# Kernel optimization log

Hardware: AMD Instinct MI355X
Metric: run time of the kernel (lower is better)

The kernel has to match this reference:

```python
import jax, jax.numpy as jnp
import numpy as np

W_, H_, D_ = 45, 30, 13
TEXT = 226
NVID = W_ * H_ * D_            # 17550 video tokens
L = TEXT + NVID                # 17776 total tokens
BLK = 128
NKEEP = 32
NBLK = (L + BLK - 1) // BLK    # 139 blocks
LPAD = NBLK * BLK              # 17792
LEVELS = (1, 2, 4, 8)
MASK_RATIOS = ((1, 0.0, 0.05), (2, 0.05, 0.15), (4, 0.15, 0.25), (8, 0.25, 0.5), (0, 0.5, 1.0))
NEG = -1e30

def _sgn(x):
    return (x > 0) - (x < 0)

def _gen3d(x, y, z, ax, ay, az, bx, by, bz, cx, cy, cz):
    w = abs(ax + ay + az); h = abs(bx + by + bz); d = abs(cx + cy + cz)
    dax, day, daz = _sgn(ax), _sgn(ay), _sgn(az)
    dbx, dby, dbz = _sgn(bx), _sgn(by), _sgn(bz)
    dcx, dcy, dcz = _sgn(cx), _sgn(cy), _sgn(cz)
    if h == 1 and d == 1:
        for _ in range(w):
            yield (x, y, z); x += dax; y += day; z += daz
        return
    if w == 1 and d == 1:
        for _ in range(h):
            yield (x, y, z); x += dbx; y += dby; z += dbz
        return
    if w == 1 and h == 1:
        for _ in range(d):
            yield (x, y, z); x += dcx; y += dcy; z += dcz
        return
    ax2, ay2, az2 = ax // 2, ay // 2, az // 2
    bx2, by2, bz2 = bx // 2, by // 2, bz // 2
    cx2, cy2, cz2 = cx // 2, cy // 2, cz // 2
    w2 = abs(ax2 + ay2 + az2); h2 = abs(bx2 + by2 + bz2); d2 = abs(cx2 + cy2 + cz2)
    if (w2 % 2) and (w > 2): ax2 += dax; ay2 += day; az2 += daz
    if (h2 % 2) and (h > 2): bx2 += dbx; by2 += dby; bz2 += dbz
    if (d2 % 2) and (d > 2): cx2 += dcx; cy2 += dcy; cz2 += dcz
    if (2 * w > 3 * h) and (2 * w > 3 * d):
        yield from _gen3d(x, y, z, ax2, ay2, az2, bx, by, bz, cx, cy, cz)
        yield from _gen3d(x + ax2, y + ay2, z + az2, ax - ax2, ay - ay2, az - az2, bx, by, bz, cx, cy, cz)
    elif 3 * h > 4 * d:
        yield from _gen3d(x, y, z, bx2, by2, bz2, cx, cy, cz, ax2, ay2, az2)
        yield from _gen3d(x + bx2, y + by2, z + bz2, ax, ay, az, bx - bx2, by - by2, bz - bz2, cx, cy, cz)
        yield from _gen3d(x + (ax - dax) + (bx2 - dbx), y + (ay - day) + (by2 - dby), z + (az - daz) + (bz2 - dbz), -bx2, -by2, -bz2, cx, cy, cz, -(ax - ax2), -(ay - ay2), -(az - az2))
    elif 3 * d > 4 * h:
        yield from _gen3d(x, y, z, cx2, cy2, cz2, ax2, ay2, az2, bx, by, bz)
        yield from _gen3d(x + cx2, y + cy2, z + cz2, ax, ay, az, bx, by, bz, cx - cx2, cy - cy2, cz - cz2)
        yield from _gen3d(x + (ax - dax) + (cx2 - dcx), y + (ay - day) + (cy2 - dcy), z + (az - daz) + (cz2 - dcz), -cx2, -cy2, -cz2, -(ax - ax2), -(ay - ay2), -(az - az2), bx, by, bz)
    else:
        yield from _gen3d(x, y, z, bx2, by2, bz2, cx2, cy2, cz2, ax2, ay2, az2)
        yield from _gen3d(x + bx2, y + by2, z + bz2, cx, cy, cz, ax2, ay2, az2, bx - bx2, by - by2, bz - bz2)
        yield from _gen3d(x + (bx2 - dbx) + (cx - dcx), y + (by2 - dby) + (cy - dcy), z + (bz2 - dbz) + (cz - dcz), ax, ay, az, -bx2, -by2, -bz2, -(cx - cx2), -(cy - cy2), -(cz - cz2))
        yield from _gen3d(x + (ax - dax) + bx2 + (cx - dcx), y + (ay - day) + by2 + (cy - dcy), z + (az - daz) + bz2 + (cz - dcz), -cx, -cy, -cz, -(ax - ax2), -(ay - ay2), -(az - az2), bx - bx2, by - by2, bz - bz2)

def _gilbert3d(w, h, d):
    if w >= h and w >= d:
        yield from _gen3d(0, 0, 0, w, 0, 0, 0, h, 0, 0, 0, d)
    elif h >= w and h >= d:
        yield from _gen3d(0, 0, 0, 0, h, 0, w, 0, 0, 0, 0, d)
    else:
        yield from _gen3d(0, 0, 0, 0, 0, d, w, 0, 0, 0, h, 0)

def _perms():
    o2g = np.zeros(NVID, np.int64); g2o = np.zeros(NVID, np.int64)
    for g, (x, y, z) in enumerate(_gilbert3d(W_, H_, D_)):
        c = x + W_ * (y + H_ * z)
        o2g[g] = c; g2o[c] = g
    return jnp.asarray(o2g), jnp.asarray(g2o)

O2G, G2O = _perms()

def _sample(x, key):
    # random_sample_tokens: same NKEEP indices (per b,h) reused for every block
    B, Hh, _, Dd = x.shape
    r = jax.random.uniform(key, (B, Hh, BLK))
    idx = jax.lax.top_k(r, NKEEP)[1]                    # [B,H,NKEEP]
    xb = x.reshape(B, Hh, NBLK, BLK, Dd)
    s = jnp.take_along_axis(xb, idx[:, :, None, :, None], axis=3)
    return s.reshape(B, Hh, NBLK * NKEEP, Dd)

def _make_mask(q, k):
    # torch.no_grad() mask path
    q = jax.lax.stop_gradient(q); k = jax.lax.stop_gradient(k)
    pad = LPAD - L
    qp = jnp.pad(q, ((0, 0), (0, 0), (0, pad), (0, 0)), mode='edge')
    kp = jnp.pad(k, ((0, 0), (0, 0), (0, pad), (0, 0)), mode='edge')
    kq, kk = jax.random.split(jax.random.key(0))
    sq = _sample(qp, kq); sk = _sample(kp, kk)
    scale = 1.0 / float(np.sqrt(q.shape[-1]))
    attn = jax.nn.softmax(jnp.einsum('bhid,bhjd->bhij', sq, sk) * scale, axis=-1)
    B, Hh = attn.shape[:2]
    # sum-pool NKEEP x NKEEP -> block-level pooled attention [B,H,NBLK,NBLK]
    pool = attn.reshape(B, Hh, NBLK, NKEEP, NBLK, NKEEP).sum(axis=(3, 5))
    # rank of each column within its row (descending) == scatter over sorted indices
    rank = jnp.argsort(jnp.argsort(-pool, axis=-1), axis=-1)
    mask = jnp.zeros(pool.shape, jnp.int32)
    for val, s, e in MASK_RATIOS:
        si = max(0, int(NBLK * s)); ei = min(NBLK, int(NBLK * e))
        if si < ei and val != 0:
            mask = jnp.where((rank >= si) & (rank < ei), jnp.int32(val), mask)
    mask = mask.at[:, :, :, -2:].set(1)
    mask = mask.at[:, :, -2:, :].set(1)
    return mask

def _pooled_kv(kp, vp):
    # per-level mean-pooled K/V per key block, padded to BLK slots + log-count bias
    B, Hh, _, Dd = kp.shape
    valid = (jnp.arange(LPAD) < L).astype(kp.dtype).reshape(NBLK, BLK)
    kb = kp.reshape(B, Hh, NBLK, BLK, Dd)
    vb = vp.reshape(B, Hh, NBLK, BLK, Dd)
    Ks, Vs, Bs = [], [], []
    for m in LEVELS:
        g = BLK // m
        cnt = valid.reshape(NBLK, g, m).sum(-1)          # [NBLK,g] valid tokens per group
        den = jnp.maximum(cnt, 1.0)
        kpl = kb.reshape(B, Hh, NBLK, g, m, Dd).sum(4) / den[None, None, :, :, None]
        vpl = vb.reshape(B, Hh, NBLK, g, m, Dd).sum(4) / den[None, None, :, :, None]
        bias = jnp.where(cnt > 0, jnp.log(den), NEG)
        padn = BLK - g
        Ks.append(jnp.pad(kpl, ((0, 0), (0, 0), (0, 0), (0, padn), (0, 0))))
        Vs.append(jnp.pad(vpl, ((0, 0), (0, 0), (0, 0), (0, padn), (0, 0))))
        Bs.append(jnp.pad(bias, ((0, 0), (0, padn)), constant_values=NEG))
    return jnp.stack(Ks, 3), jnp.stack(Vs, 3), jnp.stack(Bs, 1)

def _sparse_attn(q, k, v, mask):
    B, Hh, _, Dd = q.shape
    pad = LPAD - L
    zp = ((0, 0), (0, 0), (0, pad), (0, 0))
    qp = jnp.pad(q, zp); kp = jnp.pad(k, zp); vp = jnp.pad(v, zp)
    KL, VL, BIAS = _pooled_kv(kp, vp)   # [B,H,NBLK,4,BLK,D], bias [NBLK,4,BLK]
    table = np.zeros(9, np.int32)
    table[1], table[2], table[4], table[8] = 0, 1, 2, 3
    lvl = jnp.asarray(table)[mask]
    act = mask > 0
    scale = 1.0 / float(np.sqrt(Dd))
    qb = jnp.transpose(qp.reshape(B, Hh, NBLK, BLK, Dd), (2, 0, 1, 3, 4))
    lvl_t = jnp.transpose(lvl, (2, 0, 1, 3))
    act_t = jnp.transpose(act, (2, 0, 1, 3))
    biasB = jnp.broadcast_to(BIAS[None, None], (B, Hh, NBLK, len(LEVELS), BLK))
    def body(carry, xs):
        qi, li, ai = xs                 # [B,H,BLK,D], [B,H,NBLK], [B,H,NBLK]
        sel = li[:, :, :, None, None]
        Ksel = jnp.take_along_axis(KL, sel[..., None], axis=3)[:, :, :, 0]   # [B,H,NBLK,BLK,D]
        Vsel = jnp.take_along_axis(VL, sel[..., None], axis=3)[:, :, :, 0]
        bsel = jnp.take_along_axis(biasB, sel, axis=3)[:, :, :, 0]           # [B,H,NBLK,BLK]
        logit = jnp.einsum('bhqd,bhknd->bhqkn', qi, Ksel) * scale
        logit = logit + jnp.where(ai[:, :, None, :, None], bsel[:, :, None], NEG)
        p = jax.nn.softmax(logit.reshape(B, Hh, BLK, NBLK * BLK), axis=-1)
        o = jnp.einsum('bhqn,bhnd->bhqd', p, Vsel.reshape(B, Hh, NBLK * BLK, Dd))
        return carry, o
    body = jax.checkpoint(body)
    _, outs = jax.lax.scan(body, None, (qb, lvl_t, act_t))
    out = jnp.transpose(outs, (1, 2, 0, 3, 4)).reshape(B, Hh, LPAD, Dd)
    return out[:, :, :L]

def _forward(q, k, v):
    def rearr(x):
        return jnp.concatenate([x[:, :, TEXT:][:, :, O2G], x[:, :, :TEXT]], axis=2)
    qr, kr, vr = rearr(q), rearr(k), rearr(v)
    mask = _make_mask(qr, kr)
    outr = _sparse_attn(qr, kr, vr, mask)
    return jnp.concatenate([outr[:, :, -TEXT:], outr[:, :, :-TEXT][:, :, G2O]], axis=2)

def setup_inputs():
    key = jax.random.key(0)
    kq, kk, kv = jax.random.split(key, 3)
    shp = (1, 8, L, 64)
    return {'q': jax.random.normal(kq, shp, jnp.float32),
            'k': jax.random.normal(kk, shp, jnp.float32),
            'v': jax.random.normal(kv, shp, jnp.float32)}

def reference(q, k, v):
    return _forward(q, k, v)
```

## Files before the change

### kernel.cpp

```cpp
#include <hip/hip_runtime.h>
#include <stdint.h>
#include <string.h>
#include <stdlib.h>

#define JAX_PARTITIONABLE 1

namespace {

constexpr int kW = 45, kH = 30, kD = 13;
constexpr int NVID = kW * kH * kD;
constexpr int TEXT = 226;
constexpr int LSEQ = TEXT + NVID;
constexpr int BLKSZ = 128;
constexpr int NBLK = 139;
constexpr int LPAD = NBLK * BLKSZ;
constexpr int NKEEP = 32;
constexpr int NS = NBLK * NKEEP;
constexpr int NH = 8;
constexpr int DD = 64;
constexpr int VLAST = LSEQ - (NBLK - 1) * BLKSZ;
constexpr float SCALE = 0.125f;
constexpr float LN2F = 0.69314718055994530942f;
constexpr int MAXG = 188;

constexpr int NSPLIT = 16;
constexpr int HCHUNK = (LSEQ + 63) / 64;
constexpr int CHPER = (HCHUNK + NSPLIT - 1) / NSPLIT;
constexpr int NHEAVYB = NH * 2 * NSPLIT;
constexpr int NLIGHT = NH * (NBLK - 2);

constexpr long SZ_R  = (long)NH * LPAD * DD;
constexpr long SZ_RB = SZ_R / 2;
constexpr long SZ_SH = (long)NH * NS * DD / 2;
constexpr long SZ_PL = (long)NH * NBLK * NBLK;
constexpr long SZ_KPB = (long)NH * NBLK * 112 * DD / 2;
constexpr long SZ_O  = (long)NH * LSEQ * DD;
constexpr long SZ_PT = (long)NH * 2 * NSPLIT * BLKSZ * DD;
constexpr long SZ_PS = (long)NH * 2 * NSPLIT * BLKSZ;
constexpr long F_QR = 0;
constexpr long F_KR = F_QR + SZ_R;
constexpr long F_QB = F_KR + SZ_R;
constexpr long F_KB = F_QB + SZ_RB;
constexpr long F_VB = F_KB + SZ_RB;
constexpr long F_SQH = F_VB + SZ_RB;
constexpr long F_SQM = F_SQH + SZ_SH;
constexpr long F_SQL = F_SQM + SZ_SH;
constexpr long F_SKH = F_SQL + SZ_SH;
constexpr long F_SKM = F_SKH + SZ_SH;
constexpr long F_SKL = F_SKM + SZ_SH;
constexpr long F_PL = F_SKL + SZ_SH;
constexpr long F_KPB = F_PL + SZ_PL;
constexpr long F_VPB = F_KPB + SZ_KPB;
constexpr long F_MK = F_VPB + SZ_KPB;
constexpr long F_OR = F_MK + SZ_PL;
constexpr long F_PT = F_OR + SZ_O;
constexpr long F_PS = F_PT + SZ_PT;
constexpr long F_TB = F_PS + SZ_PS;
constexpr int TAB_INTS = 2 * LSEQ + 2 * NH * NKEEP;

struct Gil { int* out; int n; };
static inline int sgn_i(int v) { return (v > 0) - (v < 0); }
static inline int fd2(int a) { return a >= 0 ? a / 2 : -((-a + 1) / 2); }

static void gen3d(Gil& G, int x, int y, int z,
                  int ax, int ay, int az,
                  int bx, int by, int bz,
                  int cx, int cy, int cz) {
  int w = abs(ax + ay + az), h = abs(bx + by + bz), d = abs(cx + cy + cz);
  int dax = sgn_i(ax), day = sgn_i(ay), daz = sgn_i(az);
  int dbx = sgn_i(bx), dby = sgn_i(by), dbz = sgn_i(bz);
  int dcx = sgn_i(cx), dcy = sgn_i(cy), dcz = sgn_i(cz);
  if (h == 1 && d == 1) { for (int i = 0; i < w; i++) { G.out[G.n++] = x + kW * (y + kH * z); x += dax; y += day; z += daz; } return; }
  if (w == 1 && d == 1) { for (int i = 0; i < h; i++) { G.out[G.n++] = x + kW * (y + kH * z); x += dbx; y += dby; z += dbz; } return; }
  if (w == 1 && h == 1) { for (int i = 0; i < d; i++) { G.out[G.n++] = x + kW * (y + kH * z); x += dcx; y += dcy; z += dcz; } return; }
  int ax2 = fd2(ax), ay2 = fd2(ay), az2 = fd2(az);
  int bx2 = fd2(bx), by2 = fd2(by), bz2 = fd2(bz);
  int cx2 = fd2(cx), cy2 = fd2(cy), cz2 = fd2(cz);
  int w2 = abs(ax2 + ay2 + az2), h2 = abs(bx2 + by2 + bz2), d2 = abs(cx2 + cy2 + cz2);
  if ((w2 & 1) && w > 2) { ax2 += dax; ay2 += day; az2 += daz; }
  if ((h2 & 1) && h > 2) { bx2 += dbx; by2 += dby; bz2 += dbz; }
  if ((d2 & 1) && d > 2) { cx2 += dcx; cy2 += dcy; cz2 += dcz; }
  if (2 * w > 3 * h && 2 * w > 3 * d) {
    gen3d(G, x, y, z, ax2, ay2, az2, bx, by, bz, cx, cy, cz);
    gen3d(G, x + ax2, y + ay2, z + az2, ax - ax2, ay - ay2, az - az2, bx, by, bz, cx, cy, cz);
  } else if (3 * h > 4 * d) {
    gen3d(G, x, y, z, bx2, by2, bz2, cx, cy, cz, ax2, ay2, az2);
    gen3d(G, x + bx2, y + by2, z + bz2, ax, ay, az, bx - bx2, by - by2, bz - bz2, cx, cy, cz);
    gen3d(G, x + (ax - dax) + (bx2 - dbx), y + (ay - day) + (by2 - dby), z + (az - daz) + (bz2 - dbz),
          -bx2, -by2, -bz2, cx, cy, cz, -(ax - ax2), -(ay - ay2), -(az - az2));
  } else if (3 * d > 4 * h) {
    gen3d(G, x, y, z, cx2, cy2, cz2, ax2, ay2, az2, bx, by, bz);
    gen3d(G, x + cx2, y + cy2, z + cz2, ax, ay, az, bx, by, bz, cx - cx2, cy - cy2, cz - cz2);
    gen3d(G, x + (ax - dax) + (cx2 - dcx), y + (ay - day) + (cy2 - dcy), z + (az - daz) + (cz2 - dcz),
          -cx2, -cy2, -cz2, -(ax - ax2), -(ay - ay2), -(az - az2), bx, by, bz);
  } else {
    gen3d(G, x, y, z, bx2, by2, bz2, cx2, cy2, cz2, ax2, ay2, az2);
    gen3d(G, x + bx2, y + by2, z + bz2, cx, cy, cz, ax2, ay2, az2, bx - bx2, by - by2, bz - bz2);
    gen3d(G, x + (bx2 - dbx) + (cx - dcx), y + (by2 - dby) + (cy - dcy), z + (bz2 - dbz) + (cz - dcz),
          ax, ay, az, -bx2, -by2, -bz2, -(cx - cx2), -(cy - cy2), -(cz - cz2));
    gen3d(G, x + (ax - dax) + bx2 + (cx - dcx), y + (ay - day) + by2 + (cy - dcy), z + (az - daz) + bz2 + (cz - dcz),
          -cx, -cy, -cz, -(ax - ax2), -(ay - ay2), -(az - az2), bx - bx2, by - by2, bz - bz2);
  }
}

static void tf2x32(uint32_t k0, uint32_t k1, uint32_t x0, uint32_t x1,
                   uint32_t& o0, uint32_t& o1) {
// ... 59 lines not shown
  Gil G{yields, 0};
  gen3d(G, 0, 0, 0, kW, 0, 0, 0, kH, 0, 0, 0, kD);
  int n = G.n;
  if (n > NVID) n = NVID;
  for (int g = 0; g < n; g++) o2g_buf[g] = yields[g];
  for (int g = 0; g < n; g++) g2o_buf[yields[g]] = g;

  int* inmap = tab;
  int* outg  = tab + LSEQ;
  for (int g = 0; g < NVID; g++) inmap[g] = TEXT + o2g_buf[g];
  for (int t = 0; t < TEXT; t++) inmap[NVID + t] = t;
  for (int r = 0; r < TEXT; r++) outg[r] = NVID + r;
  for (int c = 0; c < NVID; c++) outg[TEXT + c] = g2o_buf[c];

  uint32_t kq0, kq1, kk0, kk1;
#if JAX_PARTITIONABLE
  tf2x32(0, 0, 0, 0, kq0, kq1);
  tf2x32(0, 0, 0, 1, kk0, kk1);
#else
  {
    uint32_t y00, y10, y01, y11;
    tf2x32(0, 0, 0, 2, y00, y10);
    tf2x32(0, 0, 1, 3, y01, y11);
    kq0 = y00; kq1 = y01; kk0 = y10; kk1 = y11;
  }
#endif
  fill_idx(kq0, kq1, tab + 2 * LSEQ);
  fill_idx(kk0, kk1, tab + 2 * LSEQ + NH * NKEEP);
}

}


typedef __attribute__((ext_vector_type(8))) short short8v;
typedef __attribute__((ext_vector_type(4))) float f32x4;

static __device__ inline unsigned short f2bf(float f) {
  unsigned u = __float_as_uint(f);
  unsigned r = u + 0x7FFFu + ((u >> 16) & 1u);
  return (unsigned short)(r >> 16);
}
static __device__ inline float bf2f(unsigned short s) {
  return __uint_as_float(((unsigned)s) << 16);
}
static __device__ inline int cvtpk(float lo, float hi) {
  int r;
  asm("v_cvt_pk_bf16_f32 %0, %1, %2" : "=v"(r) : "v"(lo), "v"(hi));
  return r;
}

struct KFrag {
  short8v h[2][2], m[2][2], l[2][2];
};


__global__ __launch_bounds__(256) void k_rearr(
    const float* __restrict__ q, const float* __restrict__ k, const float* __restrict__ v,
    float* __restrict__ qr, float* __restrict__ kr,
    short* __restrict__ qrb, short* __restrict__ krb, short* __restrict__ vrb,
    const int* __restrict__ inmap) {
  long rid = (long)blockIdx.x * 4 + (threadIdx.x >> 6);
  int d = threadIdx.x & 63;
  const long total = 3L * NH * LPAD;
  if (rid >= total) return;
  int tsel = (int)(rid / ((long)NH * LPAD));
  long rem = rid - (long)tsel * NH * LPAD;
  int h = (int)(rem / LPAD);
  int i = (int)(rem % LPAD);
  const float* src = tsel == 0 ? q : (tsel == 1 ? k : v);
  float val = 0.f;
  if (i < LSEQ) val = src[((long)h * LSEQ + inmap[i]) * DD + d];
  long o = ((long)h * LPAD + i) * DD + d;
  if (tsel == 0) { qr[o] = val; qrb[o] = (short)f2bf(val); }
  else if (tsel == 1) { kr[o] = val; krb[o] = (short)f2bf(val); }
  else { vrb[o] = (short)f2bf(val); }
}

__global__ __launch_bounds__(256) void k_sample(
    const float* __restrict__ qr, const float* __restrict__ kr,
    short* __restrict__ sqh, short* __restrict__ sqm, short* __restrict__ sql,
    short* __restrict__ skh, short* __restrict__ skm, short* __restrict__ skl,
    const int* __restrict__ qidx, const int* __restrict__ kidx) {
  long gid = (long)blockIdx.x * 256 + threadIdx.x;
  int g = (int)(gid & 7);
  long rowid = gid >> 3;
  const long half = (long)NH * NS;
  if (rowid >= 2 * half) return;
  int tsel = rowid >= half;
  long rem = tsel ? rowid - half : rowid;
  int h = (int)(rem / NS);
  int s = (int)(rem % NS);
  int b = s / NKEEP, t = s % NKEEP;
  const int* idx = tsel ? kidx : qidx;
  int p = b * BLKSZ + idx[h * NKEEP + t];
  if (p >= LSEQ) p = LSEQ - 1;
  const float* src = (tsel ? kr : qr) + ((long)h * LPAD + p) * DD + g * 8;
  float4 a = *(const float4*)src;
  float4 bb = *(const float4*)(src + 4);
  float vals[8] = {a.x, a.y, a.z, a.w, bb.x, bb.y, bb.z, bb.w};
  short8v vh, vm, vl;
#pragma unroll
  for (int j = 0; j < 8; j++) {
    unsigned short hi = f2bf(vals[j]);
    float r1 = vals[j] - bf2f(hi);
    unsigned short mi = f2bf(r1);
    float r2 = r1 - bf2f(mi);
    unsigned short lo = f2bf(r2);
    vh[j] = (short)hi; vm[j] = (short)mi; vl[j] = (short)lo;
  }
  int t16 = s >> 4, lm = s & 15, ks = g >> 2, lg = g & 3;
  long off = (long)h * NS * DD + ((long)(t16 * 2 + ks)) * 512 + (lg * 16 + lm) * 8;
  if (tsel) {
    *(short8v*)(skh + off) = vh;
    *(short8v*)(skm + off) = vm;
    *(short8v*)(skl + off) = vl;
  } else {
    *(short8v*)(sqh + off) = vh;
    *(short8v*)(sqm + off) = vm;
    *(short8v*)(sql + off) = vl;
  }
}

static __device__ inline void ld_frags(
    const short* __restrict__ skh, const short* __restrict__ skm,
    const short* __restrict__ skl, long kbase, int c, int lane, KFrag& F) {
#pragma unroll
  for (int nt = 0; nt < 2; nt++)
#pragma unroll
    for (int ks = 0; ks < 2; ks++) {
      long a = kbase + ((long)((2 * c + nt) * 2 + ks)) * 512 + lane * 8;
      F.h[nt][ks] = *(const short8v*)(skh + a);
      F.m[nt][ks] = *(const short8v*)(skm + a);
      F.l[nt][ks] = *(const short8v*)(skl + a);
    }
}

__global__ __launch_bounds__(256, 2) void k_scores_pool(
    const short* __restrict__ sqh, const short* __restrict__ sqm, const short* __restrict__ sql,
    const short* __restrict__ skh, const short* __restrict__ skm, const short* __restrict__ skl,
    float* __restrict__ pool) {
  __shared__ float bins[32][145];
  __shared__ float invden[32];
  int bid = blockIdx.x;
  int h = bid & 7, qb = bid >> 3;
  int tid = threadIdx.x;
  int wid = tid >> 6, lane = tid & 63;
  int lm = lane & 15, lg = lane >> 4;

  for (int i = tid; i < 32 * 145; i += 256) (&bins[0][0])[i] = 0.f;
// ... 67 lines not shown
  }
}

__global__ __launch_bounds__(192) void k_mask(
    const float* __restrict__ pool, int* __restrict__ mask) {
  __shared__ float row[NBLK];
  int h = blockIdx.x / NBLK, i = blockIdx.x % NBLK;
  int t = threadIdx.x;
  const float* pr = pool + ((long)h * NBLK + i) * NBLK;
  if (t < NBLK) row[t] = pr[t];
  __syncthreads();
  if (t < NBLK) {
    float pv = row[t];
    int rank = 0;
    for (int j = 0; j < NBLK; j++) {
      float o = row[j];
      rank += (o > pv) || (o == pv && j < t);
    }
    int val = 0;
    if (rank < 6) val = 1;
    else if (rank < 20) val = 2;
    else if (rank < 34) val = 4;
    else if (rank < 69) val = 8;
    if (t >= NBLK - 2) val = 1;
    if (i >= NBLK - 2) val = 1;
    mask[((long)h * NBLK + i) * NBLK + t] = val;
  }
}

__global__ __launch_bounds__(256) void k_poolkv(
    const short* __restrict__ krb, const short* __restrict__ vrb,
    short* __restrict__ Kpb, short* __restrict__ Vpb) {
  long rid = (long)blockIdx.x * 4 + (threadIdx.x >> 6);
  int d = threadIdx.x & 63;
  const long total = 2L * NH * NBLK * 112;
  if (rid >= total) return;
  int tsel = (int)(rid / ((long)NH * NBLK * 112));
  long rem = rid - (long)tsel * NH * NBLK * 112;
  int h = (int)(rem / (NBLK * 112));
  int rem2 = (int)(rem % (NBLK * 112));
  int j = rem2 / 112, p = rem2 % 112;
  int m, g;
  if (p < 64) { m = 2; g = p; }
  else if (p < 96) { m = 4; g = p - 64; }
  else { m = 8; g = p - 96; }
  const short* src = tsel ? vrb : krb;
  const short* base = src + ((long)h * LPAD + j * BLKSZ + g * m) * DD + d;
  float sum = 0.f;
  for (int r2 = 0; r2 < m; r2++) sum += bf2f((unsigned short)base[(long)r2 * DD]);
  short* dst = tsel ? Vpb : Kpb;
  dst[(((long)h * NBLK + j) * 112 + p) * DD + d] = (short)f2bf(sum / (float)m);
}

__global__ __launch_bounds__(256, 1) void k_attn_light(
    const short* __restrict__ qrb, const short* __restrict__ krb,
    const short* __restrict__ vrb,
    const short* __restrict__ Kpb, const short* __restrict__ Vpb,
    const int* __restrict__ mask,
    float* __restrict__ outr) {
  __shared__ int glist[MAXG];
  __shared__ int ngarr[NBLK + 1];
  __shared__ __align__(16) short Kt[64 * 64];
  __shared__ __align__(16) short Vt[64 * 68];
  __shared__ int smeta;

  int bid = blockIdx.x;
  int h = bid / (NBLK - 2);
  int qi = bid % (NBLK - 2);
  int tid = threadIdx.x;

  int myng = 0, mylvl = 0, myG = 0;
  if (tid < NBLK) {
    int mv = mask[((long)h * NBLK + qi) * NBLK + tid];
    if (mv) {
      mylvl = (mv == 1) ? 0 : (mv == 2) ? 1 : (mv == 4) ? 2 : 3;
      myG = ((tid == NBLK - 1) ? VLAST : BLKSZ) >> mylvl;
      myng = (myG + 15) >> 4;
    }
    ngarr[tid] = myng;
  }
  __syncthreads();
  if (tid == 0) {
    int run = 0;
    for (int j = 0; j < NBLK; j++) { int t2 = ngarr[j]; ngarr[j] = run; run += t2; }
    int tot = run;
    while (tot & 3) glist[tot++] = 0;
    smeta = tot >> 2;
  }
  __syncthreads();
  if (tid < NBLK && myng) {
    int off = ngarr[tid];
    int src0, pooled;
    if (mylvl == 0) { src0 = h * LPAD + tid * BLKSZ; pooled = 0; }
    else {
      int loff = (mylvl == 1) ? 0 : (mylvl == 2) ? 64 : 96;
      src0 = (h * NBLK + tid) * 112 + loff; pooled = 1;
    }
    for (int g = 0; g < myng; g++) {
      int cnt = myG - 16 * g; if (cnt > 16) cnt = 16;
      glist[off + g] = (src0 + 16 * g) | (cnt << 24) | (mylvl << 29) | (pooled << 31);
    }
  }

  int lane = tid & 63, wid = tid >> 6;
  int lm = lane & 15, lg = lane >> 4;

  short8v Qf[2][2];
#pragma unroll
  for (int mt = 0; mt < 2; mt++)
#pragma unroll
    for (int ks = 0; ks < 2; ks++) {
      long row = (long)h * LPAD + qi * BLKSZ + wid * 32 + mt * 16 + lm;
      Qf[mt][ks] = *(const short8v*)(qrb + row * DD + ks * 32 + lg * 8);
    }

  f32x4 Oacc[4][2];
#pragma unroll
  for (int a = 0; a < 4; a++)
#pragma unroll
    for (int b = 0; b < 2; b++) { f32x4 z = {0.f, 0.f, 0.f, 0.f}; Oacc[a][b] = z; }
  float lrow0 = 0.f, lrow1 = 0.f;

  __syncthreads();
  int nchunks = smeta;

  int sr = tid & 63;
  int sd0 = (tid >> 6) * 16;

  short8v pkA, pkB, pvA, pvB;
  {
    unsigned e = (unsigned)glist[(sr >> 4)];
    long src = (long)((e & 0xFFFFFFu) + (sr & 15));
    const short* kb = (e >> 31) ? Kpb : krb;
    const short* vb = (e >> 31) ? Vpb : vrb;
    const short8v* kp = (const short8v*)(kb + src * DD + sd0);
    const short8v* vp = (const short8v*)(vb + src * DD + sd0);
    pkA = kp[0]; pkB = kp[1];
    pvA = vp[0]; pvB = vp[1];
  }

  for (int c = 0; c < nchunks; c++) {
    __syncthreads();
    {
      int sw = (sr & 7) << 3;
      *(short8v*)&Kt[sr * 64 + (sd0 ^ sw)] = pkA;
      *(short8v*)&Kt[sr * 64 + ((sd0 + 8) ^ sw)] = pkB;
#pragma unroll
      for (int i = 0; i < 8; i++) {
        Vt[(sd0 + i) * 68 + sr] = pvA[i];
        Vt[(sd0 + 8 + i) * 68 + sr] = pvB[i];
      }
    }
    __syncthreads();
    if (c + 1 < nchunks) {
      unsigned e = (unsigned)glist[4 * (c + 1) + (sr >> 4)];
      long src = (long)((e & 0xFFFFFFu) + (sr & 15));
      const short* kb = (e >> 31) ? Kpb : krb;
      const short* vb = (e >> 31) ? Vpb : vrb;
      const short8v* kp = (const short8v*)(kb + src * DD + sd0);
      const short8v* vp = (const short8v*)(vb + src * DD + sd0);
      pkA = kp[0]; pkB = kp[1];
      pvA = vp[0]; pvB = vp[1];
    }

    int cntv[4]; float biasv[4];
#pragma unroll
    for (int g = 0; g < 4; g++) {
      unsigned e = (unsigned)glist[4 * c + g];
      cntv[g] = (e >> 24) & 31;
      biasv[g] = (float)((e >> 29) & 3) * LN2F;
    }
    bool allfull = (cntv[0] == 16) & (cntv[1] == 16) & (cntv[2] == 16) & (cntv[3] == 16);

    short8v Kf[4][2];
#pragma unroll
    for (int nt = 0; nt < 4; nt++)
#pragma unroll
      for (int ks = 0; ks < 2; ks++)
        Kf[nt][ks] = *(short8v*)&Kt[(nt * 16 + lm) * 64 + ((ks * 32 + lg * 8) ^ ((lm & 7) << 3))];

    short8v Pf[2][2];
#pragma unroll
    for (int mt = 0; mt < 2; mt++) {
      f32x4 aq[4];
#pragma unroll
      for (int nt = 0; nt < 4; nt++) {
        f32x4 z = {0.f, 0.f, 0.f, 0.f};
        f32x4 a = __builtin_amdgcn_mfma_f32_16x16x32_bf16(Kf[nt][0], Qf[mt][0], z, 0, 0, 0);
        aq[nt] = __builtin_amdgcn_mfma_f32_16x16x32_bf16(Kf[nt][1], Qf[mt][1], a, 0, 0, 0);
      }
      float ps[16];
      if (allfull) {
#pragma unroll
        for (int nt = 0; nt < 4; nt++)
#pragma unroll
          for (int i = 0; i < 4; i++)
            ps[nt * 4 + i] = __expf(fmaf(aq[nt][i], SCALE, biasv[nt]));
      } else {
#pragma unroll
        for (int nt = 0; nt < 4; nt++)
#pragma unroll
          for (int i = 0; i < 4; i++) {
            int kvr = lg * 4 + i;
            ps[nt * 4 + i] = (kvr < cntv[nt]) ? __expf(fmaf(aq[nt][i], SCALE, biasv[nt])) : 0.f;
          }
      }
      float lsum = 0.f;
#pragma unroll
      for (int i = 0; i < 16; i++) lsum += ps[i];
      if (mt == 0) lrow0 += lsum; else lrow1 += lsum;
#pragma unroll
      for (int H = 0; H < 2; H++) {
        union { int i[4]; short8v v; } u;
        u.i[0] = cvtpk(ps[8 * H + 0], ps[8 * H + 1]);
        u.i[1] = cvtpk(ps[8 * H + 2], ps[8 * H + 3]);
        u.i[2] = cvtpk(ps[8 * H + 4], ps[8 * H + 5]);
        u.i[3] = cvtpk(ps[8 * H + 6], ps[8 * H + 7]);
        Pf[mt][H] = u.v;
      }
    }

#pragma unroll
    for (int mtp = 0; mtp < 4; mtp++) {
      int d68 = (mtp * 16 + lm) * 68;
#pragma unroll
      for (int H = 0; H < 2; H++) {
        short4 lo = *(short4*)&Vt[d68 + H * 32 + lg * 4];
        short4 hi = *(short4*)&Vt[d68 + H * 32 + 16 + lg * 4];
        short8v vf;
        vf[0] = lo.x; vf[1] = lo.y; vf[2] = lo.z; vf[3] = lo.w;
        vf[4] = hi.x; vf[5] = hi.y; vf[6] = hi.z; vf[7] = hi.w;
        Oacc[mtp][0] = __builtin_amdgcn_mfma_f32_16x16x32_bf16(vf, Pf[0][H], Oacc[mtp][0], 0, 0, 0);
        Oacc[mtp][1] = __builtin_amdgcn_mfma_f32_16x16x32_bf16(vf, Pf[1][H], Oacc[mtp][1], 0, 0, 0);
      }
    }
  }

  lrow0 += __shfl_xor(lrow0, 16); lrow0 += __shfl_xor(lrow0, 32);
  lrow1 += __shfl_xor(lrow1, 16); lrow1 += __shfl_xor(lrow1, 32);
  float inv0 = 1.0f / lrow0, inv1 = 1.0f / lrow1;
#pragma unroll
  for (int mt = 0; mt < 2; mt++) {
    int grow = qi * BLKSZ + wid * 32 + mt * 16 + lm;
    float inv = mt ? inv1 : inv0;
    float* orow = outr + ((long)h * LSEQ + grow) * DD;
#pragma unroll
    for (int mtp = 0; mtp < 4; mtp++) {
      f32x4 o = Oacc[mtp][mt];
      *(float4*)(orow + mtp * 16 + lg * 4) =
          make_float4(o[0] * inv, o[1] * inv, o[2] * inv, o[3] * inv);
    }
  }
}

__global__ __launch_bounds__(256, 1) void k_attn_heavy(
    const short* __restrict__ qrb, const short* __restrict__ krb,
    const short* __restrict__ vrb,
    float* __restrict__ part, float* __restrict__ plsum) {
  __shared__ __align__(16) short Kt[64 * 64];
  __shared__ __align__(16) short Vt[64 * 68];

  int bid = blockIdx.x;
  int split = bid & (NSPLIT - 1);
  int hq = bid / NSPLIT;
  int h = hq >> 1;
  int qi = NBLK - 2 + (hq & 1);
  int c0 = split * CHPER;
  int c1 = c0 + CHPER; if (c1 > HCHUNK) c1 = HCHUNK;
  int slot = hq * NSPLIT + split;
  int tid = threadIdx.x;

  int lane = tid & 63, wid = tid >> 6;
  int lm = lane & 15, lg = lane >> 4;

  short8v Qf[2][2];
#pragma unroll
  for (int mt = 0; mt < 2; mt++)
#pragma unroll
    for (int ks = 0; ks < 2; ks++) {
      long row = (long)h * LPAD + qi * BLKSZ + wid * 32 + mt * 16 + lm;
      Qf[mt][ks] = *(const short8v*)(qrb + row * DD + ks * 32 + lg * 8);
    }

  f32x4 Oacc[4][2];
#pragma unroll
  for (int a = 0; a < 4; a++)
#pragma unroll
    for (int b = 0; b < 2; b++) { f32x4 z = {0.f, 0.f, 0.f, 0.f}; Oacc[a][b] = z; }
// ... 128 lines not shown
  int t = threadIdx.x;
  int row = t >> 1;
  int dbase = (t & 1) * 32;
  float l = 0.f;
  for (int s = 0; s < NSPLIT; s++) l += plsum[(long)(hq * NSPLIT + s) * BLKSZ + row];
  int grow = qi * BLKSZ + row;
  if (grow >= LSEQ) return;
  float inv = 1.0f / l;
  float* orow = outr + ((long)h * LSEQ + grow) * DD;
  for (int d = dbase; d < dbase + 32; d += 4) {
    float4 acc = make_float4(0.f, 0.f, 0.f, 0.f);
    for (int s = 0; s < NSPLIT; s++) {
      float4 p4 = *(const float4*)&part[((long)(hq * NSPLIT + s) * BLKSZ + row) * DD + d];
      acc.x += p4.x; acc.y += p4.y; acc.z += p4.z; acc.w += p4.w;
    }
    *(float4*)(orow + d) = make_float4(acc.x * inv, acc.y * inv, acc.z * inv, acc.w * inv);
  }
}

__global__ __launch_bounds__(256) void k_out(
    const float* __restrict__ outr, const int* __restrict__ outg,
    float* __restrict__ out) {
  long rid = (long)blockIdx.x * 4 + (threadIdx.x >> 6);
  int d = threadIdx.x & 63;
  const long total = (long)NH * LSEQ;
  if (rid >= total) return;
  int h = (int)(rid / LSEQ);
  int r = (int)(rid % LSEQ);
  int src = outg[r];
  out[((long)h * LSEQ + r) * DD + d] = outr[((long)h * LSEQ + src) * DD + d];
}


extern "C" void kernel_launch(void* const* d_in, const int* in_sizes, int n_in,
                              void* d_out, int out_size, void* d_ws, size_t ws_size,
                              hipStream_t stream) {
  (void)in_sizes; (void)n_in; (void)out_size; (void)ws_size;
  const float* q = (const float*)d_in[0];
  const float* k = (const float*)d_in[1];
  const float* v = (const float*)d_in[2];
  float* ws = (float*)d_ws;
  float* out = (float*)d_out;

  static int* htab = nullptr;
  if (!htab) { (void)hipHostMalloc((void**)&htab, TAB_INTS * sizeof(int)); }
  build_tables(htab);

  int* dtab = (int*)(ws + F_TB);
  int* inmap = dtab;
  int* outg = dtab + LSEQ;
  int* qidx = dtab + 2 * LSEQ;
  int* kidx = qidx + NH * NKEEP;
  int* dmask = (int*)(ws + F_MK);
  float* qr = ws + F_QR; float* kr = ws + F_KR;
  short* qrb = (short*)(ws + F_QB);
  short* krb = (short*)(ws + F_KB);
  short* vrb = (short*)(ws + F_VB);
  short* sqh = (short*)(ws + F_SQH);
  short* sqm = (short*)(ws + F_SQM);
  short* sql = (short*)(ws + F_SQL);
  short* skh = (short*)(ws + F_SKH);
  short* skm = (short*)(ws + F_SKM);
  short* skl = (short*)(ws + F_SKL);
  float* pool = ws + F_PL;
  short* Kpb = (short*)(ws + F_KPB);
  short* Vpb = (short*)(ws + F_VPB);
  float* outr = ws + F_OR;
  float* part = ws + F_PT;
  float* plsum = ws + F_PS;

  hipMemcpyAsync(dtab, htab, TAB_INTS * sizeof(int), hipMemcpyHostToDevice, stream);

  {
    long rows = 3L * NH * LPAD;
    k_rearr<<<dim3((unsigned)((rows + 3) / 4)), 256, 0, stream>>>(
        q, k, v, qr, kr, qrb, krb, vrb, inmap);
  }
  {
    long thr = 2L * NH * NS * 8;
    k_sample<<<dim3((unsigned)((thr + 255) / 256)), 256, 0, stream>>>(
        qr, kr, sqh, sqm, sql, skh, skm, skl, qidx, kidx);
  }
  k_scores_pool<<<dim3(NH * NBLK), 256, 0, stream>>>(
      sqh, sqm, sql, skh, skm, skl, pool);
  k_mask<<<dim3(NH * NBLK), 192, 0, stream>>>(pool, dmask);
  {
    long rows = 2L * NH * NBLK * 112;
    k_poolkv<<<dim3((unsigned)((rows + 3) / 4)), 256, 0, stream>>>(krb, vrb, Kpb, Vpb);
  }
  k_attn_heavy<<<dim3(NHEAVYB), 256, 0, stream>>>(qrb, krb, vrb, part, plsum);
  k_attn_light<<<dim3(NLIGHT), 256, 0, stream>>>(qrb, krb, vrb, Kpb, Vpb, dmask, outr);
  k_combine<<<dim3(NH * 2), 256, 0, stream>>>(part, plsum, outr);
  {
    long rows = (long)NH * LSEQ;
    k_out<<<dim3((unsigned)((rows + 3) / 4)), 256, 0, stream>>>(outr, outg, out);
  }
}
```

Before: 509.1 us.

## Pre-swizzle K/V into MFMA fragment layout and drop LDS staging in light attention

Adds two kernels that rewrite the raw and pooled bf16 K/V into per-16-row MFMA fragment order, so the light attention kernel reads fragments straight from global memory into registers. This removes the shared-memory tiles and the per-chunk barriers, and K loads are double-buffered across chunks. Occupancy is raised to two blocks per CU, the fp32 rearranged Q/K buffers are dropped (sampling now reads the original inputs through inmap), rearrangement is vectorised, and exp is folded into exp2 with a pre-scaled constant. The cost is two extra launches and a full extra copy of K/V in HBM, and the V reads are gathers.

```diff
diff --git a/kernel.cpp b/kernel.cpp
--- a/kernel.cpp
+++ b/kernel.cpp
@@ -20,8 +20,14 @@
 constexpr int DD = 64;
 constexpr int VLAST = LSEQ - (NBLK - 1) * BLKSZ;
 constexpr float SCALE = 0.125f;
+constexpr float SC2 = 0.18033688011120542f;
 constexpr float LN2F = 0.69314718055994530942f;
 constexpr int MAXG = 188;
+
+constexpr int NGR_H = LPAD / 16;
+constexpr int NRAWG = NH * NGR_H;
+constexpr int NPOOLG = NH * NBLK * 7;
+constexpr int NGALL = NRAWG + NPOOLG;
 
 constexpr int NSPLIT = 16;
 constexpr int HCHUNK = (LSEQ + 63) / 64;
@@ -29,17 +35,16 @@
 constexpr int NHEAVYB = NH * 2 * NSPLIT;
 constexpr int NLIGHT = NH * (NBLK - 2);
 
-constexpr long SZ_R  = (long)NH * LPAD * DD;
-constexpr long SZ_RB = SZ_R / 2;
+constexpr long SZ_RB = (long)NH * LPAD * DD / 2;
 constexpr long SZ_SH = (long)NH * NS * DD / 2;
+constexpr long SZ_KPB = (long)NH * NBLK * 112 * DD / 2;
+constexpr long SZ_KF = (long)NGALL * 1024 / 2;
+constexpr long SZ_VF = (long)NGALL * 1024 / 2;
 constexpr long SZ_PL = (long)NH * NBLK * NBLK;
-constexpr long SZ_KPB = (long)NH * NBLK * 112 * DD / 2;
 constexpr long SZ_O  = (long)NH * LSEQ * DD;
 constexpr long SZ_PT = (long)NH * 2 * NSPLIT * BLKSZ * DD;
 constexpr long SZ_PS = (long)NH * 2 * NSPLIT * BLKSZ;
-constexpr long F_QR = 0;
-constexpr long F_KR = F_QR + SZ_R;
-constexpr long F_QB = F_KR + SZ_R;
+constexpr long F_QB = 0;
 constexpr long F_KB = F_QB + SZ_RB;
 constexpr long F_VB = F_KB + SZ_RB;
 constexpr long F_SQH = F_VB + SZ_RB;
@@ -48,10 +53,12 @@
 constexpr long F_SKH = F_SQL + SZ_SH;
 constexpr long F_SKM = F_SKH + SZ_SH;
 constexpr long F_SKL = F_SKM + SZ_SH;
-constexpr long F_PL = F_SKL + SZ_SH;
-constexpr long F_KPB = F_PL + SZ_PL;
+constexpr long F_KPB = F_SKL + SZ_SH;
 constexpr long F_VPB = F_KPB + SZ_KPB;
-constexpr long F_MK = F_VPB + SZ_KPB;
+constexpr long F_KFA = F_VPB + SZ_KPB;
+constexpr long F_VFA = F_KFA + SZ_KF;
+constexpr long F_PL = F_VFA + SZ_VF;
+constexpr long F_MK = F_PL + SZ_PL;
 constexpr long F_OR = F_MK + SZ_PL;
 constexpr long F_PT = F_OR + SZ_O;
 constexpr long F_PS = F_PT + SZ_PT;
@@ -217,35 +224,47 @@
 struct KFrag {
   short8v h[2][2], m[2][2], l[2][2];
 };
+struct KF2 {
+  short8v k[4][2];
+};
 
 
 __global__ __launch_bounds__(256) void k_rearr(
     const float* __restrict__ q, const float* __restrict__ k, const float* __restrict__ v,
-    float* __restrict__ qr, float* __restrict__ kr,
     short* __restrict__ qrb, short* __restrict__ krb, short* __restrict__ vrb,
     const int* __restrict__ inmap) {
-  long rid = (long)blockIdx.x * 4 + (threadIdx.x >> 6);
-  int d = threadIdx.x & 63;
-  const long total = 3L * NH * LPAD;
-  if (rid >= total) return;
-  int tsel = (int)(rid / ((long)NH * LPAD));
-  long rem = rid - (long)tsel * NH * LPAD;
+  long gid = (long)blockIdx.x * 256 + threadIdx.x;
+  const long totalRows = 3L * NH * LPAD;
+  long rowid = gid >> 3;
+  int g8 = (int)(gid & 7);
+  if (rowid >= totalRows) return;
+  int tsel = (int)(rowid / ((long)NH * LPAD));
+  long rem = rowid - (long)tsel * NH * LPAD;
   int h = (int)(rem / LPAD);
   int i = (int)(rem % LPAD);
   const float* src = tsel == 0 ? q : (tsel == 1 ? k : v);
-  float val = 0.f;
-  if (i < LSEQ) val = src[((long)h * LSEQ + inmap[i]) * DD + d];
-  long o = ((long)h * LPAD + i) * DD + d;
-  if (tsel == 0) { qr[o] = val; qrb[o] = (short)f2bf(val); }
-  else if (tsel == 1) { kr[o] = val; krb[o] = (short)f2bf(val); }
-  else { vrb[o] = (short)f2bf(val); }
+  short8v outv;
+  if (i < LSEQ) {
+    const float* sp = src + ((long)h * LSEQ + inmap[i]) * DD + g8 * 8;
+    float4 a = *(const float4*)sp;
+    float4 b = *(const float4*)(sp + 4);
+    float vals[8] = {a.x, a.y, a.z, a.w, b.x, b.y, b.z, b.w};
+#pragma unroll
+    for (int j = 0; j < 8; j++) outv[j] = (short)f2bf(vals[j]);
+  } else {
+#pragma unroll
+    for (int j = 0; j < 8; j++) outv[j] = 0;
+  }
+  short* dst = tsel == 0 ? qrb : (tsel == 1 ? krb : vrb);
+  *(short8v*)(dst + ((long)h * LPAD + i) * DD + g8 * 8) = outv;
 }
 
 __global__ __launch_bounds__(256) void k_sample(
-    const float* __restrict__ qr, const float* __restrict__ kr,
+    const float* __restrict__ q, const float* __restrict__ k,
     short* __restrict__ sqh, short* __restrict__ sqm, short* __restrict__ sql,
     short* __restrict__ skh, short* __restrict__ skm, short* __restrict__ skl,
-    const int* __restrict__ qidx, const int* __restrict__ kidx) {
+    const int* __restrict__ qidx, const int* __restrict__ kidx,
+    const int* __restrict__ inmap) {
   long gid = (long)blockIdx.x * 256 + threadIdx.x;
   int g = (int)(gid & 7);
   long rowid = gid >> 3;
@@ -259,7 +278,8 @@
   const int* idx = tsel ? kidx : qidx;
   int p = b * BLKSZ + idx[h * NKEEP + t];
   if (p >= LSEQ) p = LSEQ - 1;
-  const float* src = (tsel ? kr : qr) + ((long)h * LPAD + p) * DD + g * 8;
+  int orig = inmap[p];
+  const float* src = (tsel ? k : q) + ((long)h * LSEQ + orig) * DD + g * 8;
   float4 a = *(const float4*)src;
   float4 bb = *(const float4*)(src + 4);
   float vals[8] = {a.x, a.y, a.z, a.w, bb.x, bb.y, bb.z, bb.w};
@@ -433,22 +453,60 @@
   dst[(((long)h * NBLK + j) * 112 + p) * DD + d] = (short)f2bf(sum / (float)m);
 }
 
-__global__ __launch_bounds__(256, 1) void k_attn_light(
-    const short* __restrict__ qrb, const short* __restrict__ krb,
-    const short* __restrict__ vrb,
-    const short* __restrict__ Kpb, const short* __restrict__ Vpb,
+__global__ __launch_bounds__(256) void k_fragk(
+    const short* __restrict__ krb, const short* __restrict__ Kpb,
+    short* __restrict__ kfAll) {
+  long gid = (long)blockIdx.x * 256 + threadIdx.x;
+  if (gid >= (long)NGALL * 128) return;
+  int lane = (int)(gid & 63);
+  int ks = (int)((gid >> 6) & 1);
+  long grp = gid >> 7;
+  int lm = lane & 15, lg = lane >> 4;
+  const short* srcp;
+  long row;
+  if (grp < NRAWG) { srcp = krb; row = grp * 16 + lm; }
+  else { srcp = Kpb; row = (grp - NRAWG) * 16 + lm; }
+  short8v vv = *(const short8v*)(srcp + row * DD + ks * 32 + lg * 8);
+  *(short8v*)(kfAll + ((long)grp * 2 + ks) * 512 + lane * 8) = vv;
+}
+
+__global__ __launch_bounds__(256) void k_fragv(
+    const short* __restrict__ vrb, const short* __restrict__ Vpb,
+    short* __restrict__ vfAll) {
+  long gid = (long)blockIdx.x * 256 + threadIdx.x;
+  if (gid >= (long)NGALL * 256) return;
+  int lane = (int)(gid & 63);
+  int mtp = (int)((gid >> 6) & 3);
+  long grp = gid >> 8;
+  int lm = lane & 15, lg = lane >> 4;
+  const short* srcp;
+  long rowb;
+  if (grp < NRAWG) { srcp = vrb; rowb = grp * 16 + lg * 4; }
+  else { srcp = Vpb; rowb = (grp - NRAWG) * 16 + lg * 4; }
+  short4 o;
+  o.x = srcp[(rowb + 0) * DD + mtp * 16 + lm];
+  o.y = srcp[(rowb + 1) * DD + mtp * 16 + lm];
+  o.z = srcp[(rowb + 2) * DD + mtp * 16 + lm];
+  o.w = srcp[(rowb + 3) * DD + mtp * 16 + lm];
+  *(short4*)(vfAll + ((long)grp * 4 + mtp) * 256 + lane * 4) = o;
+}
+
+__global__ __launch_bounds__(256, 2) void k_attn_light(
+    const short* __restrict__ qrb,
+    const short* __restrict__ kfAll, const short* __restrict__ vfAll,
     const int* __restrict__ mask,
     float* __restrict__ outr) {
   __shared__ int glist[MAXG];
-  __shared__ int ngarr[NBLK + 1];
-  __shared__ __align__(16) short Kt[64 * 64];
-  __shared__ __align__(16) short Vt[64 * 68];
+  __shared__ int ngarr[NBLK];
+  __shared__ int wtot[4];
   __shared__ int smeta;
 
   int bid = blockIdx.x;
   int h = bid / (NBLK - 2);
   int qi = bid % (NBLK - 2);
   int tid = threadIdx.x;
+  int lane = tid & 63, wid = tid >> 6;
+  int lm = lane & 15, lg = lane >> 4;
 
   int myng = 0, mylvl = 0, myG = 0;
   if (tid < NBLK) {
@@ -458,33 +516,40 @@
       myG = ((tid == NBLK - 1) ? VLAST : BLKSZ) >> mylvl;
       myng = (myG + 15) >> 4;
     }
-    ngarr[tid] = myng;
-  }
+  }
+  int v = myng;
+#pragma unroll
+  for (int off = 1; off < 64; off <<= 1) {
+    int t2 = __shfl_up(v, off);
+    if ((tid & 63) >= off) v += t2;
+  }
+  if ((tid & 63) == 63) wtot[wid] = v;
   __syncthreads();
+  int woff = 0;
+#pragma unroll
+  for (int w = 0; w < 4; w++) if (w < wid) woff += wtot[w];
+  if (tid < NBLK) ngarr[tid] = woff + v - myng;
   if (tid == 0) {
-    int run = 0;
-    for (int j = 0; j < NBLK; j++) { int t2 = ngarr[j]; ngarr[j] = run; run += t2; }
-    int tot = run;
+    int tot = wtot[0] + wtot[1] + wtot[2] + wtot[3];
     while (tot & 3) glist[tot++] = 0;
     smeta = tot >> 2;
   }
   __syncthreads();
   if (tid < NBLK && myng) {
     int off = ngarr[tid];
-    int src0, pooled;
-    if (mylvl == 0) { src0 = h * LPAD + tid * BLKSZ; pooled = 0; }
+    int grp0;
+    if (mylvl == 0) grp0 = h * NGR_H + tid * 8;
     else {
-      int loff = (mylvl == 1) ? 0 : (mylvl == 2) ? 64 : 96;
-      src0 = (h * NBLK + tid) * 112 + loff; pooled = 1;
+      int l16 = (mylvl == 1) ? 0 : (mylvl == 2) ? 4 : 6;
+      grp0 = NRAWG + (h * NBLK + tid) * 7 + l16;
     }
     for (int g = 0; g < myng; g++) {
       int cnt = myG - 16 * g; if (cnt > 16) cnt = 16;
-      glist[off + g] = (src0 + 16 * g) | (cnt << 24) | (mylvl << 29) | (pooled << 31);
-    }
-  }
-
-  int lane = tid & 63, wid = tid >> 6;
-  int lm = lane & 15, lg = lane >> 4;
+      glist[off + g] = (grp0 + g) | (cnt << 24) | (mylvl << 29);
+    }
+  }
+  __syncthreads();
+  int nchunks = smeta;
 
   short8v Qf[2][2];
 #pragma unroll
@@ -502,63 +567,32 @@
     for (int b = 0; b < 2; b++) { f32x4 z = {0.f, 0.f, 0.f, 0.f}; Oacc[a][b] = z; }
   float lrow0 = 0.f, lrow1 = 0.f;
 
-  __syncthreads();
-  int nchunks = smeta;
-
-  int sr = tid & 63;
-  int sd0 = (tid >> 6) * 16;
-
-  short8v pkA, pkB, pvA, pvB;
-  {
-    unsigned e = (unsigned)glist[(sr >> 4)];
-    long src = (long)((e & 0xFFFFFFu) + (sr & 15));
-    const short* kb = (e >> 31) ? Kpb : krb;
-    const short* vb = (e >> 31) ? Vpb : vrb;
-    const short8v* kp = (const short8v*)(kb + src * DD + sd0);
-    const short8v* vp = (const short8v*)(vb + src * DD + sd0);
-    pkA = kp[0]; pkB = kp[1];
-    pvA = vp[0]; pvB = vp[1];
-  }
-
-  for (int c = 0; c < nchunks; c++) {
-    __syncthreads();
-    {
-      int sw = (sr & 7) << 3;
-      *(short8v*)&Kt[sr * 64 + (sd0 ^ sw)] = pkA;
-      *(short8v*)&Kt[sr * 64 + ((sd0 + 8) ^ sw)] = pkB;
-#pragma unroll
-      for (int i = 0; i < 8; i++) {
-        Vt[(sd0 + i) * 68 + sr] = pvA[i];
-        Vt[(sd0 + 8 + i) * 68 + sr] = pvB[i];
-      }
-    }
-    __syncthreads();
-    if (c + 1 < nchunks) {
-      unsigned e = (unsigned)glist[4 * (c + 1) + (sr >> 4)];
-      long src = (long)((e & 0xFFFFFFu) + (sr & 15));
-      const short* kb = (e >> 31) ? Kpb : krb;
-      const short* vb = (e >> 31) ? Vpb : vrb;
-      const short8v* kp = (const short8v*)(kb + src * DD + sd0);
-      const short8v* vp = (const short8v*)(vb + src * DD + sd0);
-      pkA = kp[0]; pkB = kp[1];
-      pvA = vp[0]; pvB = vp[1];
-    }
-
-    int cntv[4]; float biasv[4];
+  auto ldK = [&](int c, KF2& F) {
+#pragma unroll
+    for (int g = 0; g < 4; g++) {
+      long grp = (long)((unsigned)glist[4 * c + g] & 0xFFFFFFu);
+#pragma unroll
+      for (int ks = 0; ks < 2; ks++)
+        F.k[g][ks] = *(const short8v*)(kfAll + (grp * 2 + ks) * 512 + lane * 8);
+    }
+  };
+
+  auto doChunk = [&](const KF2& F, int c) {
+    int cntv[4]; float biasv[4]; long grpv[4];
 #pragma unroll
     for (int g = 0; g < 4; g++) {
       unsigned e = (unsigned)glist[4 * c + g];
+      grpv[g] = (long)(e & 0xFFFFFFu);
       cntv[g] = (e >> 24) & 31;
-      biasv[g] = (float)((e >> 29) & 3) * LN2F;
-    }
+      biasv[g] = (float)((e >> 29) & 3);
+    }
+    short4 Vfr[4][4];
+#pragma unroll
+    for (int g = 0; g < 4; g++)
+#pragma unroll
+      for (int mtp = 0; mtp < 4; mtp++)
+        Vfr[g][mtp] = *(const short4*)(vfAll + (grpv[g] * 4 + mtp) * 256 + lane * 4);
     bool allfull = (cntv[0] == 16) & (cntv[1] == 16) & (cntv[2] == 16) & (cntv[3] == 16);
-
-    short8v Kf[4][2];
-#pragma unroll
-    for (int nt = 0; nt < 4; nt++)
-#pragma unroll
-      for (int ks = 0; ks < 2; ks++)
-        Kf[nt][ks] = *(short8v*)&Kt[(nt * 16 + lm) * 64 + ((ks * 32 + lg * 8) ^ ((lm & 7) << 3))];
 
     short8v Pf[2][2];
 #pragma unroll
@@ -567,8 +601,8 @@
 #pragma unroll
       for (int nt = 0; nt < 4; nt++) {
         f32x4 z = {0.f, 0.f, 0.f, 0.f};
-        f32x4 a = __builtin_amdgcn_mfma_f32_16x16x32_bf16(Kf[nt][0], Qf[mt][0], z, 0, 0, 0);
-        aq[nt] = __builtin_amdgcn_mfma_f32_16x16x32_bf16(Kf[nt][1], Qf[mt][1], a, 0, 0, 0);
+        f32x4 a = __builtin_amdgcn_mfma_f32_16x16x32_bf16(F.k[nt][0], Qf[mt][0], z, 0, 0, 0);
+        aq[nt] = __builtin_amdgcn_mfma_f32_16x16x32_bf16(F.k[nt][1], Qf[mt][1], a, 0, 0, 0);
       }
       float ps[16];
       if (allfull) {
@@ -576,14 +610,14 @@
         for (int nt = 0; nt < 4; nt++)
 #pragma unroll
           for (int i = 0; i < 4; i++)
-            ps[nt * 4 + i] = __expf(fmaf(aq[nt][i], SCALE, biasv[nt]));
+            ps[nt * 4 + i] = exp2f(fmaf(aq[nt][i], SC2, biasv[nt]));
       } else {
 #pragma unroll
         for (int nt = 0; nt < 4; nt++)
 #pragma unroll
           for (int i = 0; i < 4; i++) {
             int kvr = lg * 4 + i;
-            ps[nt * 4 + i] = (kvr < cntv[nt]) ? __expf(fmaf(aq[nt][i], SCALE, biasv[nt])) : 0.f;
+            ps[nt * 4 + i] = (kvr < cntv[nt]) ? exp2f(fmaf(aq[nt][i], SC2, biasv[nt])) : 0.f;
           }
       }
       float lsum = 0.f;
@@ -600,21 +634,27 @@
         Pf[mt][H] = u.v;
       }
     }
-
-#pragma unroll
-    for (int mtp = 0; mtp < 4; mtp++) {
-      int d68 = (mtp * 16 + lm) * 68;
+#pragma unroll
+    for (int mtp = 0; mtp < 4; mtp++)
 #pragma unroll
       for (int H = 0; H < 2; H++) {
-        short4 lo = *(short4*)&Vt[d68 + H * 32 + lg * 4];
-        short4 hi = *(short4*)&Vt[d68 + H * 32 + 16 + lg * 4];
+        short4 lo = Vfr[2 * H][mtp], hi = Vfr[2 * H + 1][mtp];
         short8v vf;
         vf[0] = lo.x; vf[1] = lo.y; vf[2] = lo.z; vf[3] = lo.w;
         vf[4] = hi.x; vf[5] = hi.y; vf[6] = hi.z; vf[7] = hi.w;
         Oacc[mtp][0] = __builtin_amdgcn_mfma_f32_16x16x32_bf16(vf, Pf[0][H], Oacc[mtp][0], 0, 0, 0);
         Oacc[mtp][1] = __builtin_amdgcn_mfma_f32_16x16x32_bf16(vf, Pf[1][H], Oacc[mtp][1], 0, 0, 0);
       }
-    }
+  };
+
+  KF2 A, B;
+  ldK(0, A);
+  for (int c = 0; c < nchunks; c += 2) {
+    if (c + 1 < nchunks) ldK(c + 1, B);
+    doChunk(A, c);
+    if (c + 1 >= nchunks) break;
+    if (c + 2 < nchunks) ldK(c + 2, A);
+    doChunk(B, c + 1);
   }
 
   lrow0 += __shfl_xor(lrow0, 16); lrow0 += __shfl_xor(lrow0, 32);
@@ -849,7 +889,6 @@
   int* qidx = dtab + 2 * LSEQ;
   int* kidx = qidx + NH * NKEEP;
   int* dmask = (int*)(ws + F_MK);
-  float* qr = ws + F_QR; float* kr = ws + F_KR;
   short* qrb = (short*)(ws + F_QB);
   short* krb = (short*)(ws + F_KB);
   short* vrb = (short*)(ws + F_VB);
@@ -859,9 +898,11 @@
   short* skh = (short*)(ws + F_SKH);
   short* skm = (short*)(ws + F_SKM);
   short* skl = (short*)(ws + F_SKL);
-  float* pool = ws + F_PL;
   short* Kpb = (short*)(ws + F_KPB);
   short* Vpb = (short*)(ws + F_VPB);
+  short* kfAll = (short*)(ws + F_KFA);
+  short* vfAll = (short*)(ws + F_VFA);
+  float* pool = ws + F_PL;
   float* outr = ws + F_OR;
   float* part = ws + F_PT;
   float* plsum = ws + F_PS;
@@ -869,14 +910,14 @@
   hipMemcpyAsync(dtab, htab, TAB_INTS * sizeof(int), hipMemcpyHostToDevice, stream);
 
   {
-    long rows = 3L * NH * LPAD;
-    k_rearr<<<dim3((unsigned)((rows + 3) / 4)), 256, 0, stream>>>(
-        q, k, v, qr, kr, qrb, krb, vrb, inmap);
+    long thr = 3L * NH * LPAD * 8;
+    k_rearr<<<dim3((unsigned)((thr + 255) / 256)), 256, 0, stream>>>(
+        q, k, v, qrb, krb, vrb, inmap);
   }
   {
     long thr = 2L * NH * NS * 8;
     k_sample<<<dim3((unsigned)((thr + 255) / 256)), 256, 0, stream>>>(
-        qr, kr, sqh, sqm, sql, skh, skm, skl, qidx, kidx);
+        q, k, sqh, sqm, sql, skh, skm, skl, qidx, kidx, inmap);
   }
   k_scores_pool<<<dim3(NH * NBLK), 256, 0, stream>>>(
       sqh, sqm, sql, skh, skm, skl, pool);
@@ -885,8 +926,16 @@
     long rows = 2L * NH * NBLK * 112;
     k_poolkv<<<dim3((unsigned)((rows + 3) / 4)), 256, 0, stream>>>(krb, vrb, Kpb, Vpb);
   }
+  {
+    long thr = (long)NGALL * 128;
+    k_fragk<<<dim3((unsigned)((thr + 255) / 256)), 256, 0, stream>>>(krb, Kpb, kfAll);
+  }
+  {
+    long thr = (long)NGALL * 256;
+    k_fragv<<<dim3((unsigned)((thr + 255) / 256)), 256, 0, stream>>>(vrb, Vpb, vfAll);
+  }
   k_attn_heavy<<<dim3(NHEAVYB), 256, 0, stream>>>(qrb, krb, vrb, part, plsum);
-  k_attn_light<<<dim3(NLIGHT), 256, 0, stream>>>(qrb, krb, vrb, Kpb, Vpb, dmask, outr);
+  k_attn_light<<<dim3(NLIGHT), 256, 0, stream>>>(qrb, kfAll, vfAll, dmask, outr);
   k_combine<<<dim3(NH * 2), 256, 0, stream>>>(part, plsum, outr);
   {
     long rows = (long)NH * LSEQ;
```

Measured after the change: 509.6 us. No clear change (+0.1%).
